# Kernel tuning notes

Hardware: AMD Instinct MI355X
Metric: run time of the kernel (lower is better)

Reference implementation:

```python
import jax, jax.numpy as jnp
import numpy as np
import math

D_MODEL = 1024
N_HEADS = 16
HEAD_DIM = D_MODEL // N_HEADS


def setup_inputs() -> dict:
    key = jax.random.key(0)
    ks = jax.random.split(key, 6)
    scale = 1.0 / math.sqrt(D_MODEL)
    x = jax.random.normal(ks[0], (4, 2048, D_MODEL), dtype=jnp.float32)
    # nn.Linear weights stored as [out, in]; we keep [in, out] for x @ W
    Wq = jax.random.uniform(ks[1], (D_MODEL, D_MODEL), jnp.float32, -scale, scale)
    Wk = jax.random.uniform(ks[2], (D_MODEL, D_MODEL), jnp.float32, -scale, scale)
    Wv = jax.random.uniform(ks[3], (D_MODEL, D_MODEL), jnp.float32, -scale, scale)
    Wo = jax.random.uniform(ks[4], (D_MODEL, D_MODEL), jnp.float32, -scale, scale)
    bo = jax.random.uniform(ks[5], (D_MODEL,), jnp.float32, -scale, scale)
    return {"x": x, "Wq": Wq, "Wk": Wk, "Wv": Wv, "Wo": Wo, "bo": bo}


def reference(x, Wq, Wk, Wv, Wo, bo):
    B, S, _ = x.shape
    H, Dh = N_HEADS, HEAD_DIM
    # project and split heads -> [B, H, S, Dh]
    q = (x @ Wq).reshape(B, S, H, Dh).transpose(0, 2, 1, 3)
    k = (x @ Wk).reshape(B, S, H, Dh).transpose(0, 2, 1, 3)
    v = (x @ Wv).reshape(B, S, H, Dh).transpose(0, 2, 1, 3)
    scores = jnp.einsum('bhqd,bhkd->bhqk', q, k) / math.sqrt(Dh)
    causal = jnp.tril(jnp.ones((S, S), dtype=bool))  # True = keep
    scores = jnp.where(causal, scores, -jnp.inf)
    attn = jax.nn.softmax(scores, axis=-1)  # dropout=0.0 -> no-op
    out = jnp.einsum('bhqk,bhkd->bhqd', attn, v)
    out = out.transpose(0, 2, 1, 3).reshape(B, S, H * Dh)
    return out @ Wo + bo
```

## Files before the change

### kernel.cpp

```cpp
#include <hip/hip_runtime.h>
#include <hip/hip_bf16.h>

#define DEV __device__ __forceinline__

typedef unsigned short u16;
typedef unsigned int u32;
typedef __bf16 bf16x8 __attribute__((ext_vector_type(8)));
typedef float f32x4 __attribute__((ext_vector_type(4)));

static constexpr int S   = 2048;
static constexpr int D   = 1024;
static constexpr int H   = 16;
static constexpr int Dh  = 64;
static constexpr int B_  = 4;
static constexpr int M   = B_ * S;

DEV u16 f2bf(float f) {
    __hip_bfloat16 h = __float2bfloat16(f);
    union { __hip_bfloat16 h; u16 u; } cv; cv.h = h; return cv.u;
}
DEV float bf2f(u16 u) {
    union { u16 u; __hip_bfloat16 h; } cv; cv.u = u; return __bfloat162float(cv.h);
}
DEV u16 f2bf_rne(float f) {
    union { float f; u32 u; } cv; cv.f = f;
    u32 u = cv.u;
    u += 0x7FFFu + ((u >> 16) & 1u);
    return (u16)(u >> 16);
}
DEV float ex2(float x) {
    float r;
    asm("v_exp_f32 %0, %1" : "=v"(r) : "v"(x));
    return r;
}
DEV f32x4 mfma16(bf16x8 a, bf16x8 b, f32x4 c) {
    return __builtin_amdgcn_mfma_f32_16x16x32_bf16(a, b, c, 0, 0, 0);
}
DEV void llds16(const u16* g, u16* l) {
    __builtin_amdgcn_global_load_lds(
        (const __attribute__((address_space(1))) u32*)g,
        (__attribute__((address_space(3))) u32*)l, 16, 0, 0);
}
DEV bf16x8 ld8f(const float* p) {
    const f32x4* q = reinterpret_cast<const f32x4*>(p);
    f32x4 a = q[0], b = q[1];
    union { u16 u[8]; bf16x8 v; } r;
    r.u[0] = f2bf(a[0]); r.u[1] = f2bf(a[1]); r.u[2] = f2bf(a[2]); r.u[3] = f2bf(a[3]);
    r.u[4] = f2bf(b[0]); r.u[5] = f2bf(b[1]); r.u[6] = f2bf(b[2]); r.u[7] = f2bf(b[3]);
    return r.v;
}

__global__ __launch_bounds__(256) void prep(
    const float* __restrict__ x,
    const float* __restrict__ Wq, const float* __restrict__ Wk,
    const float* __restrict__ Wv, const float* __restrict__ Wo,
    u16* __restrict__ WT, u16* __restrict__ xb)
{
    const int z = blockIdx.z;
    const int tid = threadIdx.x;
    __shared__ u16 T[64 * 72];
    if (z < 4) {
        const float* src = z == 0 ? Wq : z == 1 ? Wk : z == 2 ? Wv : Wo;
        u16* dst = WT + (size_t)z * D * D;
        const int k0 = blockIdx.x * 64, n0 = blockIdx.y * 64;
        for (int c = tid; c < 512; c += 256) {
            int r = c >> 3, cc = (c & 7) << 3;
            *reinterpret_cast<bf16x8*>(&T[r * 72 + cc]) =
                ld8f(&src[(size_t)(k0 + r) * D + n0 + cc]);
        }
        __syncthreads();
        for (int c = tid; c < 512; c += 256) {
            int r = c >> 3, cc = (c & 7) << 3;
            u16 tmp[8];
            #pragma unroll
            for (int i = 0; i < 8; ++i) tmp[i] = T[(cc + i) * 72 + r];
            *reinterpret_cast<bf16x8*>(&dst[(size_t)(n0 + r) * D + k0 + cc]) =
                *reinterpret_cast<const bf16x8*>(tmp);
        }
    } else {
        size_t lin = ((size_t)(z - 4) * 256 + blockIdx.y * 16 + blockIdx.x);
        size_t i = (lin * 256 + tid) * 8;
        *reinterpret_cast<bf16x8*>(xb + i) = ld8f(x + i);
    }
}

__global__ __launch_bounds__(256) void qkv_gemm128(
    const u16* __restrict__ A, const u16* __restrict__ WT,
    u16* __restrict__ qkv, u16* __restrict__ vtb)
{
    const int bm = blockIdx.x;
    const int bn = blockIdx.y;

    __shared__ u16 SB[128 * 136];
    u16* As = SB;
    u16* Bs = SB + 8192;

    const int tid  = threadIdx.x;
    const int wave = tid >> 6, ln = tid & 63;
    const int ln15 = ln & 15, quad = ln >> 4;
    const int swz  = ln15 & 7;
    const int wm = (wave >> 1) * 64, wn = (wave & 1) * 64;

    const u16* Ab = A  + (size_t)(bm * 128) * D;
    const u16* Bb = WT + (size_t)(bn * 128) * D;

    int srow[4], soff[4];
    #pragma unroll
    for (int k = 0; k < 4; ++k) {
        int ch = wave * 256 + k * 64 + ln;
        srow[k] = ch >> 3;
        soff[k] = ((ch & 7) ^ (srow[k] & 7)) * 8;
    }

    f32x4 acc[4][4] = {};

    for (int k0 = 0; k0 < D; k0 += 64) {
        __syncthreads();
        #pragma unroll
        for (int k = 0; k < 4; ++k) {
            llds16(Ab + (size_t)srow[k] * D + k0 + soff[k], &As[(wave * 4 + k) * 512]);
            llds16(Bb + (size_t)srow[k] * D + k0 + soff[k], &Bs[(wave * 4 + k) * 512]);
        }
        __syncthreads();
        #pragma unroll
        for (int ks = 0; ks < 2; ++ks) {
            bf16x8 af[4], bfr[4];
            #pragma unroll
            for (int i = 0; i < 4; ++i)
                af[i] = *reinterpret_cast<const bf16x8*>(
                    &As[(wm + i * 16 + ln15) * 64 + ((ks * 4 + quad) ^ swz) * 8]);
            #pragma unroll
            for (int j = 0; j < 4; ++j)
                bfr[j] = *reinterpret_cast<const bf16x8*>(
                    &Bs[(wn + j * 16 + ln15) * 64 + ((ks * 4 + quad) ^ swz) * 8]);
            #pragma unroll
            for (int i = 0; i < 4; ++i)
                #pragma unroll
                for (int j = 0; j < 4; ++j)
                    acc[i][j] = mfma16(af[i], bfr[j], acc[i][j]);
        }
    }

    const int matn = bn >> 3;
    const int t0 = bm * 128, b = t0 >> 11, s0 = t0 & (S - 1);
    __syncthreads();

    if (matn < 2) {
        u16* outp = qkv + (size_t)matn * M * D;
        #pragma unroll
        for (int i = 0; i < 4; ++i)
            #pragma unroll
            for (int j = 0; j < 4; ++j)
                #pragma unroll
                for (int r = 0; r < 4; ++r)
                    SB[(wm + i * 16 + quad * 4 + r) * 136 + wn + j * 16 + ln15] =
                        f2bf(acc[i][j][r]);
        __syncthreads();
        #pragma unroll
        for (int k = 0; k < 8; ++k) {
            int c = k * 256 + tid;
            int row = c >> 4, cc = (c & 15) * 8;
            int head = (bn & 7) * 2 + (cc >> 6);
            int s = s0 + row;
            *reinterpret_cast<bf16x8*>(
                &outp[(((size_t)(b * H + head)) * S + s) * Dh + (cc & 63)]) =
                *reinterpret_cast<const bf16x8*>(&SB[row * 136 + cc]);
        }
    } else {
        #pragma unroll
        for (int h2 = 0; h2 < 2; ++h2) {
            if ((wave & 1) == h2) {
                #pragma unroll
                for (int i = 0; i < 4; ++i)
                    #pragma unroll
                    for (int j = 0; j < 4; ++j)
                        #pragma unroll
                        for (int r = 0; r < 4; ++r) {
                            int sl = wm + i * 16 + quad * 4 + r;
                            int dh = j * 16 + ln15;
                            SB[dh * 136 + sl] = f2bf(acc[i][j][r]);
                        }
            }
            __syncthreads();
            const int bh = b * H + (bn & 7) * 2 + h2;
            u16* dst = vtb + (size_t)bh * Dh * S + s0;
            for (int c = tid; c < 1024; c += 256) {
                int r = c >> 4, cc = (c & 15) * 8;
                *reinterpret_cast<bf16x8*>(&dst[(size_t)r * S + cc]) =
                    *reinterpret_cast<const bf16x8*>(&SB[r * 136 + cc]);
            }
            __syncthreads();
        }
    }
}

__global__ __launch_bounds__(256) void attn_kernel(
    const u16* __restrict__ qbuf, const u16* __restrict__ kbuf,
    const u16* __restrict__ vt, u16* __restrict__ attno)
{
    const int i  = blockIdx.x;
    const int bh = blockIdx.y;
    const int b = bh >> 4, h = bh & 15;
    const int qt[2] = {i, 31 - i};

    __shared__ u16 Ks[2][64 * 64];
    __shared__ u16 Vs[2][64 * 64];
    __shared__ u16 Ps[4][16 * 72];

    const int tid  = threadIdx.x;
    const int wave = tid >> 6, ln = tid & 63;
    const int ln15 = ln & 15, quad = ln >> 4;
    const int swz  = ln15 & 7;

    const u16* kp0 = kbuf + (size_t)bh * S * Dh;
    const u16* vp0 = vt   + (size_t)bh * Dh * S;

    bf16x8 qf[2][2];
    #pragma unroll
    for (int t = 0; t < 2; ++t) {
        const u16* qp = qbuf + ((size_t)bh * S + qt[t] * 64 + wave * 16 + ln15) * Dh;
        #pragma unroll
        for (int st = 0; st < 2; ++st) {
            union { bf16x8 v; u16 u[8]; } in, ot;
            in.v = *reinterpret_cast<const bf16x8*>(&qp[st * 32 + quad * 8]);
            #pragma unroll
            for (int k = 0; k < 8; ++k) ot.u[k] = f2bf(bf2f(in.u[k]) * 0.18033688f);
            qf[t][st] = ot.v;
        }
    }

    float l_st[2][4] = {};
    f32x4 o_st[2][4] = {};

    u16* psw = &Ps[wave][0];
    const int lrow = wave * 16 + quad * 4;

    const int c0 = wave * 128 + ln;
    const int c1 = c0 + 64;
    const int kr0 = c0 >> 3, ko0 = (((c0 & 7) ^ (kr0 & 7)) * 8);
    const int kr1 = c1 >> 3, ko1 = (((c1 & 7) ^ (kr1 & 7)) * 8);

    auto stage = [&](int kblk, int buf) {
        llds16(kp0 + ((size_t)kblk * 64 + kr0) * Dh + ko0, &Ks[buf][(wave * 2 + 0) * 512]);
        llds16(kp0 + ((size_t)kblk * 64 + kr1) * Dh + ko1, &Ks[buf][(wave * 2 + 1) * 512]);
        llds16(vp0 + (size_t)kr0 * S + kblk * 64 + ko0,    &Vs[buf][(wave * 2 + 0) * 512]);
        llds16(vp0 + (size_t)kr1 * S + kblk * 64 + ko1,    &Vs[buf][(wave * 2 + 1) * 512]);
    };

    bf16x8 kf[2][4], vf[2][4];

    auto step = [&](int t, bool domask) {
        const bf16x8* qa = qf[t];
        float* l_r = l_st[t];
        f32x4* oa = o_st[t];
        f32x4 sf[4] = {};
        #pragma unroll
        for (int j = 0; j < 4; ++j) {
            sf[j] = mfma16(qa[0], kf[0][j], sf[j]);
            sf[j] = mfma16(qa[1], kf[1][j], sf[j]);
        }
        if (domask) {
            #pragma unroll
            for (int j = 0; j < 4; ++j) {
                int kg = j * 16 + ln15;
                #pragma unroll
                for (int r = 0; r < 4; ++r)
                    if (kg > lrow + r) sf[j][r] = -3e38f;
            }
        }
        #pragma unroll
        for (int j = 0; j < 4; ++j)
            #pragma unroll
            for (int r = 0; r < 4; ++r) {
                float p = ex2(sf[j][r] - 24.0f);
                sf[j][r] = p;
                l_r[r] += p;
            }
        #pragma unroll
        for (int j = 0; j < 4; ++j)
            #pragma unroll
            for (int r = 0; r < 4; ++r)
                psw[(quad * 4 + r) * 72 + j * 16 + ln15] = f2bf_rne(sf[j][r]);

        #pragma unroll
        for (int st = 0; st < 2; ++st) {
            bf16x8 pa = *reinterpret_cast<const bf16x8*>(&psw[ln15 * 72 + st * 32 + quad * 8]);
            #pragma unroll
            for (int jd = 0; jd < 4; ++jd)
                oa[jd] = mfma16(pa, vf[st][jd], oa[jd]);
        }
    };

    const int nstage = qt[1] + 1;
    stage(0, 0);
    int cur = 0;
    for (int kblk = 0; kblk < nstage; ++kblk) {
        __syncthreads();
        if (kblk + 1 < nstage) stage(kblk + 1, cur ^ 1);
        #pragma unroll
        for (int st = 0; st < 2; ++st)
            #pragma unroll
            for (int j = 0; j < 4; ++j) {
                kf[st][j] = *reinterpret_cast<const bf16x8*>(
                    &Ks[cur][(j * 16 + ln15) * 64 + ((st * 4 + quad) ^ swz) * 8]);
                vf[st][j] = *reinterpret_cast<const bf16x8*>(
                    &Vs[cur][(j * 16 + ln15) * 64 + ((st * 4 + quad) ^ swz) * 8]);
            }
        step(1, kblk == qt[1]);
        if (kblk <= qt[0]) step(0, kblk == qt[0]);
        cur ^= 1;
    }

    #pragma unroll
    for (int t = 0; t < 2; ++t) {
        float linv[4];
        #pragma unroll
        for (int r = 0; r < 4; ++r) {
            float l = l_st[t][r];
            l += __shfl_xor(l, 1, 64);
            l += __shfl_xor(l, 2, 64);
            l += __shfl_xor(l, 4, 64);
            l += __shfl_xor(l, 8, 64);
            linv[r] = 1.0f / l;
        }
        #pragma unroll
        for (int jd = 0; jd < 4; ++jd)
            #pragma unroll
            for (int r = 0; r < 4; ++r) {
                int qrow = qt[t] * 64 + wave * 16 + quad * 4 + r;
                size_t off = ((size_t)(b * S + qrow)) * D + h * Dh + jd * 16 + ln15;
                attno[off] = f2bf(o_st[t][jd][r] * linv[r]);
            }
    }
}

__global__ __launch_bounds__(256) void proj_gemm128(
    const u16* __restrict__ A, const u16* __restrict__ WoT,
    const float* __restrict__ bo, float* __restrict__ out)
{
    const int bm = blockIdx.x;
    const int bn = blockIdx.y;

    __shared__ u16 As[8192];
    __shared__ u16 Bs[8192];

    const int tid  = threadIdx.x;
    const int wave = tid >> 6, ln = tid & 63;
    const int ln15 = ln & 15, quad = ln >> 4;
    const int swz  = ln15 & 7;
    const int wm = (wave >> 1) * 64, wn = (wave & 1) * 64;

    const u16* Ab = A   + (size_t)(bm * 128) * D;
    const u16* Bb = WoT + (size_t)(bn * 128) * D;

    int srow[4], soff[4];
    #pragma unroll
    for (int k = 0; k < 4; ++k) {
        int ch = wave * 256 + k * 64 + ln;
        srow[k] = ch >> 3;
        soff[k] = ((ch & 7) ^ (srow[k] & 7)) * 8;
    }

    f32x4 acc[4][4] = {};

    for (int k0 = 0; k0 < D; k0 += 64) {
        __syncthreads();
        #pragma unroll
        for (int k = 0; k < 4; ++k) {
            llds16(Ab + (size_t)srow[k] * D + k0 + soff[k], &As[(wave * 4 + k) * 512]);
            llds16(Bb + (size_t)srow[k] * D + k0 + soff[k], &Bs[(wave * 4 + k) * 512]);
        }
        __syncthreads();
        #pragma unroll
        for (int ks = 0; ks < 2; ++ks) {
            bf16x8 af[4], bfr[4];
            #pragma unroll
            for (int i = 0; i < 4; ++i)
                af[i] = *reinterpret_cast<const bf16x8*>(
                    &As[(wm + i * 16 + ln15) * 64 + ((ks * 4 + quad) ^ swz) * 8]);
            #pragma unroll
            for (int j = 0; j < 4; ++j)
                bfr[j] = *reinterpret_cast<const bf16x8*>(
                    &Bs[(wn + j * 16 + ln15) * 64 + ((ks * 4 + quad) ^ swz) * 8]);
            #pragma unroll
            for (int i = 0; i < 4; ++i)
                #pragma unroll
                for (int j = 0; j < 4; ++j)
                    acc[i][j] = mfma16(af[i], bfr[j], acc[i][j]);
        }
    }

    #pragma unroll
    for (int i = 0; i < 4; ++i)
        #pragma unroll
        for (int j = 0; j < 4; ++j)
            #pragma unroll
            for (int r = 0; r < 4; ++r) {
                int t   = bm * 128 + wm + i * 16 + quad * 4 + r;
                int col = bn * 128 + wn + j * 16 + ln15;
                out[(size_t)t * D + col] = acc[i][j][r] + bo[col];
            }
}

extern "C" void kernel_launch(void* const* d_in, const int* in_sizes, int n_in,
                              void* d_out, int out_size, void* d_ws, size_t ws_size,
                              hipStream_t stream) {
    const float* x  = (const float*)d_in[0];
    const float* Wq = (const float*)d_in[1];
    const float* Wk = (const float*)d_in[2];
    const float* Wv = (const float*)d_in[3];
    const float* Wo = (const float*)d_in[4];
    const float* bo = (const float*)d_in[5];
    float* out = (float*)d_out;
    u16* ws  = (u16*)d_ws;

    u16* WT   = ws;
    u16* xb   = WT + (size_t)4 * D * D;
    u16* qkvb = xb + (size_t)M * D;
    u16* kb   = qkvb + (size_t)M * D;
    u16* vtb  = qkvb + (size_t)2 * M * D;
    u16* attn = xb;

    prep        <<<dim3(16, 16, 20), 256, 0, stream>>>(x, Wq, Wk, Wv, Wo, WT, xb);
    qkv_gemm128 <<<dim3(64, 24),     256, 0, stream>>>(xb, WT, qkvb, vtb);
    attn_kernel <<<dim3(16, 64),     256, 0, stream>>>(qkvb, kb, vtb, attn);
    proj_gemm128<<<dim3(64, 8),      256, 0, stream>>>(attn, WT + (size_t)3 * D * D, bo, out);
}
```

Measured before the change: 265.1 us.

## Compute transposed scores so P feeds PV MFMA directly from registers

Result: no change. 262.4 us (-1.0%).

```diff
diff --git a/kernel.cpp b/kernel.cpp
--- a/kernel.cpp
+++ b/kernel.cpp
@@ -6,6 +6,7 @@
 typedef unsigned short u16;
 typedef unsigned int u32;
 typedef __bf16 bf16x8 __attribute__((ext_vector_type(8)));
+typedef short s16x4 __attribute__((ext_vector_type(4)));
 typedef float f32x4 __attribute__((ext_vector_type(4)));
 
 static constexpr int S   = 2048;
@@ -35,6 +36,9 @@
 }
 DEV f32x4 mfma16(bf16x8 a, bf16x8 b, f32x4 c) {
     return __builtin_amdgcn_mfma_f32_16x16x32_bf16(a, b, c, 0, 0, 0);
+}
+DEV f32x4 mfma16k(s16x4 a, s16x4 b, f32x4 c) {
+    return __builtin_amdgcn_mfma_f32_16x16x16bf16_1k(a, b, c, 0, 0, 0);
 }
 DEV void llds16(const u16* g, u16* l) {
     __builtin_amdgcn_global_load_lds(
@@ -205,7 +209,6 @@
 
     __shared__ u16 Ks[2][64 * 64];
     __shared__ u16 Vs[2][64 * 64];
-    __shared__ u16 Ps[4][16 * 72];
 
     const int tid  = threadIdx.x;
     const int wave = tid >> 6, ln = tid & 63;
@@ -229,11 +232,10 @@
         }
     }
 
-    float l_st[2][4] = {};
+    float l_st[2] = {};
     f32x4 o_st[2][4] = {};
 
-    u16* psw = &Ps[wave][0];
-    const int lrow = wave * 16 + quad * 4;
+    const int qlocal = wave * 16 + ln15;
 
     const int c0 = wave * 128 + ln;
     const int c1 = c0 + 64;
@@ -247,48 +249,36 @@
         llds16(vp0 + (size_t)kr1 * S + kblk * 64 + ko1,    &Vs[buf][(wave * 2 + 1) * 512]);
     };
 
-    bf16x8 kf[2][4], vf[2][4];
-
-    auto step = [&](int t, bool domask) {
-        const bf16x8* qa = qf[t];
-        float* l_r = l_st[t];
-        f32x4* oa = o_st[t];
+    bf16x8 kf[2][4];
+
+    auto qkphase = [&](int t, bool domask, s16x4* pa) {
         f32x4 sf[4] = {};
         #pragma unroll
         for (int j = 0; j < 4; ++j) {
-            sf[j] = mfma16(qa[0], kf[0][j], sf[j]);
-            sf[j] = mfma16(qa[1], kf[1][j], sf[j]);
+            sf[j] = mfma16(kf[0][j], qf[t][0], sf[j]);
+            sf[j] = mfma16(kf[1][j], qf[t][1], sf[j]);
         }
         if (domask) {
             #pragma unroll
             for (int j = 0; j < 4; ++j) {
-                int kg = j * 16 + ln15;
                 #pragma unroll
                 for (int r = 0; r < 4; ++r)
-                    if (kg > lrow + r) sf[j][r] = -3e38f;
-            }
-        }
-        #pragma unroll
-        for (int j = 0; j < 4; ++j)
+                    if (j * 16 + quad * 4 + r > qlocal) sf[j][r] = -3e38f;
+            }
+        }
+        float lacc = 0.0f;
+        #pragma unroll
+        for (int j = 0; j < 4; ++j) {
+            union { u16 u[4]; s16x4 v; } pk;
             #pragma unroll
             for (int r = 0; r < 4; ++r) {
                 float p = ex2(sf[j][r] - 24.0f);
-                sf[j][r] = p;
-                l_r[r] += p;
-            }
-        #pragma unroll
-        for (int j = 0; j < 4; ++j)
-            #pragma unroll
-            for (int r = 0; r < 4; ++r)
-                psw[(quad * 4 + r) * 72 + j * 16 + ln15] = f2bf_rne(sf[j][r]);
-
-        #pragma unroll
-        for (int st = 0; st < 2; ++st) {
-            bf16x8 pa = *reinterpret_cast<const bf16x8*>(&psw[ln15 * 72 + st * 32 + quad * 8]);
-            #pragma unroll
-            for (int jd = 0; jd < 4; ++jd)
-                oa[jd] = mfma16(pa, vf[st][jd], oa[jd]);
-        }
+                lacc += p;
+                pk.u[r] = f2bf_rne(p);
+            }
+            pa[j] = pk.v;
+        }
+        l_st[t] += lacc;
     };
 
     const int nstage = qt[1] + 1;
@@ -300,29 +290,44 @@
         #pragma unroll
         for (int st = 0; st < 2; ++st)
             #pragma unroll
-            for (int j = 0; j < 4; ++j) {
+            for (int j = 0; j < 4; ++j)
                 kf[st][j] = *reinterpret_cast<const bf16x8*>(
                     &Ks[cur][(j * 16 + ln15) * 64 + ((st * 4 + quad) ^ swz) * 8]);
-                vf[st][j] = *reinterpret_cast<const bf16x8*>(
-                    &Vs[cur][(j * 16 + ln15) * 64 + ((st * 4 + quad) ^ swz) * 8]);
-            }
-        step(1, kblk == qt[1]);
-        if (kblk <= qt[0]) step(0, kblk == qt[0]);
+
+        s16x4 pa1[4], pa0[4];
+        qkphase(1, kblk == qt[1], pa1);
+        const bool do0 = kblk <= qt[0];
+        if (do0) qkphase(0, kblk == qt[0], pa0);
+
+        #pragma unroll
+        for (int jd = 0; jd < 4; ++jd) {
+            s16x4 vv[4];
+            #pragma unroll
+            for (int j = 0; j < 4; ++j)
+                vv[j] = *reinterpret_cast<const s16x4*>(
+                    &Vs[cur][(jd * 16 + ln15) * 64 +
+                             ((j * 2 + (quad >> 1)) ^ swz) * 8 + (quad & 1) * 4]);
+            #pragma unroll
+            for (int j = 0; j < 4; ++j)
+                o_st[1][jd] = mfma16k(pa1[j], vv[j], o_st[1][jd]);
+            if (do0) {
+                #pragma unroll
+                for (int j = 0; j < 4; ++j)
+                    o_st[0][jd] = mfma16k(pa0[j], vv[j], o_st[0][jd]);
+            }
+        }
         cur ^= 1;
     }
 
     #pragma unroll
     for (int t = 0; t < 2; ++t) {
+        float l = l_st[t];
+        l += __shfl_xor(l, 16, 64);
+        l += __shfl_xor(l, 32, 64);
         float linv[4];
         #pragma unroll
-        for (int r = 0; r < 4; ++r) {
-            float l = l_st[t][r];
-            l += __shfl_xor(l, 1, 64);
-            l += __shfl_xor(l, 2, 64);
-            l += __shfl_xor(l, 4, 64);
-            l += __shfl_xor(l, 8, 64);
-            linv[r] = 1.0f / l;
-        }
+        for (int r = 0; r < 4; ++r)
+            linv[r] = 1.0f / __shfl(l, quad * 4 + r, 16);
         #pragma unroll
         for (int jd = 0; jd < 4; ++jd)
             #pragma unroll
```
